# Kernel optimization log

Measured on AMD Instinct MI355X. Metric: run time of the kernel, lower is better.

Reference implementation:

```python
import jax, jax.numpy as jnp
import numpy as np

B, N, D, H = 8, 1024, 1024, 16
DK = D // H


def setup_inputs() -> dict:
    key = jax.random.key(0)
    ks = jax.random.split(key, 5)
    s_in = 1.0 / np.sqrt(D)
    return {
        "x": jax.random.normal(ks[0], (B, N, D), dtype=jnp.float32),
        "w_qkv": jax.random.uniform(ks[1], (D, 3 * D), jnp.float32, -s_in, s_in),
        "b_qkv": jax.random.uniform(ks[2], (3 * D,), jnp.float32, -s_in, s_in),
        "w_proj": jax.random.uniform(ks[3], (D, D), jnp.float32, -s_in, s_in),
        "b_proj": jax.random.uniform(ks[4], (D,), jnp.float32, -s_in, s_in),
    }


def reference(x, w_qkv, b_qkv, w_proj, b_proj):
    # x: (B, N, D)
    qkv = x @ w_qkv + b_qkv                      # (B, N, 3D)
    q, k, v = jnp.split(qkv, 3, axis=-1)
    # reshape to (B, H, N, DK)
    def heads(t):
        return t.reshape(B, N, H, DK).transpose(0, 2, 1, 3)
    q, k, v = heads(q), heads(k), heads(v)
    scale = 1.0 / np.sqrt(DK).astype(np.float32)
    scores = jnp.einsum("bhnd,bhmd->bhnm", q, k) * scale  # (B, H, N, N)
    attn = jax.nn.softmax(scores, axis=-1)
    out = jnp.einsum("bhnm,bhmd->bhnd", attn, v)          # (B, H, N, DK)
    out = out.transpose(0, 2, 1, 3).reshape(B, N, D)
    return out @ w_proj + b_proj
```

## Files before the change

kernel.cpp:

```cpp
#include <hip/hip_runtime.h>
#include <hip/hip_bf16.h>


#define BB 8
#define NN 1024
#define DD 1024
#define HH 16
#define DK 64
#define TOK (BB * NN)
#define QKVN (3 * DD)

typedef __attribute__((ext_vector_type(8))) short bf16x8;
typedef __attribute__((ext_vector_type(4))) float f32x4;
typedef __attribute__((ext_vector_type(4))) short short4v;
typedef __attribute__((ext_vector_type(4))) float float4v;

static __device__ __forceinline__ short f2bf(float f) {
  union { float f; unsigned u; } v; v.f = f;
  unsigned r = (v.u + 0x7FFFu + ((v.u >> 16) & 1u)) >> 16;
  return (short)r;
}
static __device__ __forceinline__ short f2bf_rn(float f) {
  __hip_bfloat16 h(f);
  short s;
  __builtin_memcpy(&s, &h, 2);
  return s;
}
static __device__ __forceinline__ float fexp2(float x) {
#if __has_builtin(__builtin_amdgcn_exp2f)
  return __builtin_amdgcn_exp2f(x);
#else
  return __expf(x * 0.69314718056f);
#endif
}

static __device__ __forceinline__ void gload_lds16(const short* g, short* lds, int lane) {
#if __has_builtin(__builtin_amdgcn_global_load_lds)
  __builtin_amdgcn_global_load_lds((const __attribute__((address_space(1))) void*)g,
                                   (__attribute__((address_space(3))) void*)lds, 16, 0, 0);
#else
  ((bf16x8*)lds)[lane] = *(const bf16x8*)g;
#endif
}

static __device__ __forceinline__ void block_barrier() {
  asm volatile("" ::: "memory");
  __builtin_amdgcn_s_barrier();
  asm volatile("" ::: "memory");
}

__global__ __launch_bounds__(256) void cast_f32_bf16(const float* __restrict__ in,
                                                     short* __restrict__ out, long n) {
  long i = ((long)blockIdx.x * blockDim.x + threadIdx.x) * 4;
  if (i >= n) return;
  float4v v = *(const float4v*)(in + i);
  short4v o;
  o[0] = f2bf(v[0]); o[1] = f2bf(v[1]); o[2] = f2bf(v[2]); o[3] = f2bf(v[3]);
  *(short4v*)(out + i) = o;
}

__global__ __launch_bounds__(256) void transpose_cast(const float* __restrict__ in,
                                                      short* __restrict__ out,
                                                      int rows, int cols) {
  __shared__ float tile[32][33];
  int bx = blockIdx.x * 32;
  int by = blockIdx.y * 32;
  int tx = threadIdx.x, ty = threadIdx.y;
#pragma unroll
  for (int q = 0; q < 4; q++)
    tile[ty + 8 * q][tx] = in[(long)(by + ty + 8 * q) * cols + bx + tx];
  __syncthreads();
#pragma unroll
  for (int q = 0; q < 4; q++)
    out[(long)(bx + ty + 8 * q) * rows + by + tx] = f2bf(tile[tx][ty + 8 * q]);
}

__global__ __launch_bounds__(512, 2) void gemm256(const short* __restrict__ A,
                                                  const short* __restrict__ Bt,
                                                  const float* __restrict__ bias,
                                                  short* __restrict__ Cqk,
                                                  int M, int N, int K, int ldc) {
  __shared__ __align__(16) short lds[2][2][2][128 * 64];
  const int tid = threadIdx.x;
  const int wid = tid >> 6, lane = tid & 63;
  const int r = lane & 15, g = lane >> 4;
  const int wm = wid >> 2, wn = wid & 3;

  const int nwg = gridDim.x * gridDim.y;
  const int flat = blockIdx.y * gridDim.x + blockIdx.x;
  const int swz = (flat & 7) * (nwg >> 3) + (flat >> 3);
  const int bx = swz % gridDim.x, by = swz / gridDim.x;
  const long tileM = (long)by * 256, tileN = (long)bx * 256;

  f32x4 acc[8][4] = {};

  const int sc = ((lane & 7) ^ ((lane >> 3) & 7)) * 8;
  const int srl = lane >> 3;

  const int akc0 = ((0 + g) ^ (r & 7)) * 8;
  const int akc1 = ((4 + g) ^ (r & 7)) * 8;
  const int bn0 = (wn & 1) * 64;
  const int bhh = wn >> 1;

#define STAGEA(buf, h, Tt)                                                          \
  {                                                                                 \
    _Pragma("unroll") for (int j = 0; j < 2; j++)                                   \
      gload_lds16(A + (tileM + (h) * 128 + wid * 16 + j * 8 + srl) * (long)K +      \
                      (Tt) * 64 + sc,                                               \
                  &lds[buf][0][h][(wid * 2 + j) * 512], lane);                      \
  }
#define STAGEB(buf, h, Tt)                                                          \
  {                                                                                 \
    _Pragma("unroll") for (int j = 0; j < 2; j++)                                   \
      gload_lds16(Bt + (tileN + (h) * 128 + wid * 16 + j * 8 + srl) * (long)K +     \
                      (Tt) * 64 + sc,                                               \
                  &lds[buf][1][h][(wid * 2 + j) * 512], lane);                      \
  }
#define READ_A(q, p)                                                                \
  af[0][0] = *(const bf16x8*)&lds[q][0][wm][((p) * 32 + r) * 64 + akc0];            \
  af[0][1] = *(const bf16x8*)&lds[q][0][wm][((p) * 32 + r) * 64 + akc1];            \
  af[1][0] = *(const bf16x8*)&lds[q][0][wm][((p) * 32 + 16 + r) * 64 + akc0];       \
  af[1][1] = *(const bf16x8*)&lds[q][0][wm][((p) * 32 + 16 + r) * 64 + akc1];
#define READ_B(q)                                                                   \
  {                                                                                 \
    const short* Bh = &lds[q][1][bhh][0];                                           \
    _Pragma("unroll") for (int fn = 0; fn < 4; fn++) {                              \
      bf[fn][0] = *(const bf16x8*)&Bh[(bn0 + fn * 16 + r) * 64 + akc0];             \
      bf[fn][1] = *(const bf16x8*)&Bh[(bn0 + fn * 16 + r) * 64 + akc1];             \
    }                                                                               \
  }
#define WAITL()                                                                     \
  asm volatile("s_waitcnt lgkmcnt(0)" ::: "memory");                                \
  __builtin_amdgcn_sched_barrier(0);
#define MFMA_P(p)                                                                   \
  __builtin_amdgcn_s_setprio(1);                                                    \
  _Pragma("unroll") for (int fmi = 0; fmi < 2; fmi++)                               \
      _Pragma("unroll") for (int fn = 0; fn < 4; fn++) {                            \
    acc[2 * (p) + fmi][fn] = __builtin_amdgcn_mfma_f32_16x16x32_bf16(               \
        af[fmi][0], bf[fn][0], acc[2 * (p) + fmi][fn], 0, 0, 0);                    \
    acc[2 * (p) + fmi][fn] = __builtin_amdgcn_mfma_f32_16x16x32_bf16(               \
        af[fmi][1], bf[fn][1], acc[2 * (p) + fmi][fn], 0, 0, 0);                    \
  }                                                                                 \
  __builtin_amdgcn_s_setprio(0);

  const int NT = K >> 6;
  const int NIT = NT >> 1;

  STAGEA(0, 0, 0); STAGEA(0, 1, 0); STAGEB(0, 0, 0); STAGEB(0, 1, 0);
  STAGEB(1, 0, 1); STAGEB(1, 1, 1);
  asm volatile("s_waitcnt vmcnt(4)" ::: "memory");
  block_barrier();

  for (int i = 0; i < NIT; ++i) {
    const int t1 = 2 * i + 1, t2 = 2 * i + 2, t3 = 2 * i + 3;
    const bool full = (i < NIT - 1);
    bf16x8 af[2][2], bf[4][2];

    READ_A(0, 0); READ_B(0);
    STAGEA(1, 0, t1);
    block_barrier(); WAITL(); MFMA_P(0); block_barrier();

    READ_A(0, 1);
    STAGEA(1, 1, t1);
    block_barrier(); WAITL(); MFMA_P(1); block_barrier();

    READ_A(0, 2);
    if (full) STAGEB(0, 0, t2);
    block_barrier(); WAITL(); MFMA_P(2); block_barrier();

    READ_A(0, 3);
    if (full) STAGEB(0, 1, t2);
    if (full) asm volatile("s_waitcnt vmcnt(4)" ::: "memory");
    else      asm volatile("s_waitcnt vmcnt(0)" ::: "memory");
    block_barrier(); WAITL(); MFMA_P(3); block_barrier();

    READ_A(1, 0); READ_B(1);
    if (full) STAGEA(0, 0, t2);
    block_barrier(); WAITL(); MFMA_P(0); block_barrier();

    READ_A(1, 1);
    if (full) STAGEA(0, 1, t2);
    block_barrier(); WAITL(); MFMA_P(1); block_barrier();

    READ_A(1, 2);
    if (full) STAGEB(1, 0, t3);
    block_barrier(); WAITL(); MFMA_P(2); block_barrier();

    READ_A(1, 3);
    if (full) STAGEB(1, 1, t3);
    if (full) asm volatile("s_waitcnt vmcnt(4)" ::: "memory");
    block_barrier(); WAITL(); MFMA_P(3); block_barrier();
  }
#undef STAGEA
#undef STAGEB
#undef READ_A
#undef READ_B
#undef WAITL
#undef MFMA_P

#pragma unroll
  for (int fm = 0; fm < 8; fm++) {
    long rowb = tileM + wm * 128 + fm * 16 + g * 4;
#pragma unroll
    for (int fn = 0; fn < 4; fn++) {
      long cn = tileN + wn * 64 + fn * 16 + r;
      float bv = bias[cn];
      Cqk[(rowb + 0) * ldc + cn] = f2bf(acc[fm][fn][0] + bv);
      Cqk[(rowb + 1) * ldc + cn] = f2bf(acc[fm][fn][1] + bv);
      Cqk[(rowb + 2) * ldc + cn] = f2bf(acc[fm][fn][2] + bv);
      Cqk[(rowb + 3) * ldc + cn] = f2bf(acc[fm][fn][3] + bv);
    }
  }
}

template <int MODE>
__global__ __launch_bounds__(256) void gemm_bt(const short* __restrict__ A,
                                               const short* __restrict__ Bt,
                                               const float* __restrict__ bias,
                                               void* __restrict__ Cout,
                                               short* __restrict__ vT,
                                               int M, int N, int K, int ldc) {
  __shared__ __align__(16) short As[2][128 * 32];
  __shared__ __align__(16) short Bs[2][128 * 32];
  const int tid = threadIdx.x;
  const int w = tid >> 6, lane = tid & 63;
  const int r = lane & 15, g = lane >> 4;
  const int wm = w >> 1, wn = w & 1;

  const int nwg = gridDim.x * gridDim.y;
  const int flat = blockIdx.y * gridDim.x + blockIdx.x;
  const int swz = (flat & 7) * (nwg >> 3) + (flat >> 3);
  const int bx = swz % gridDim.x, by = swz / gridDim.x;

  const long tileM = (long)by * 128;
  const long tileN = (long)bx * 128;

  f32x4 acc[4][4] = {};

  const int rowInChunk = lane >> 2;
  const int colOff = ((lane & 3) ^ ((lane >> 3) & 3)) * 8;
  const int rdChunk = (g ^ ((r >> 1) & 3)) * 8;

  const int nt = K >> 5;
#pragma unroll
  for (int issue = 0; issue < 2; ++issue) {
    int c = w * 2 + issue;
    gload_lds16(A + (tileM + c * 16 + rowInChunk) * (long)K + colOff, &As[0][c * 512], lane);
    gload_lds16(Bt + (tileN + c * 16 + rowInChunk) * (long)K + colOff, &Bs[0][c * 512], lane);
  }
  __syncthreads();

  for (int t = 0; t < nt; ++t) {
    const int cur = t & 1;
    if (t + 1 < nt) {
      const int k0 = (t + 1) << 5;
#pragma unroll
      for (int issue = 0; issue < 2; ++issue) {
        int c = w * 2 + issue;
        gload_lds16(A + (tileM + c * 16 + rowInChunk) * (long)K + k0 + colOff,
                    &As[cur ^ 1][c * 512], lane);
        gload_lds16(Bt + (tileN + c * 16 + rowInChunk) * (long)K + k0 + colOff,
                    &Bs[cur ^ 1][c * 512], lane);
      }
    }

    bf16x8 a[4], b[4];
#pragma unroll
    for (int i = 0; i < 4; i++)
      a[i] = *(const bf16x8*)&As[cur][(wm * 64 + i * 16 + r) * 32 + rdChunk];
#pragma unroll
    for (int i = 0; i < 4; i++)
      b[i] = *(const bf16x8*)&Bs[cur][(wn * 64 + i * 16 + r) * 32 + rdChunk];
#pragma unroll
    for (int i = 0; i < 4; i++)
#pragma unroll
      for (int ii = 0; ii < 4; ii++)
        acc[i][ii] = __builtin_amdgcn_mfma_f32_16x16x32_bf16(a[i], b[ii], acc[i][ii], 0, 0, 0);

    __syncthreads();
  }

#pragma unroll
  for (int i = 0; i < 4; i++) {
    long rowb = tileM + wm * 64 + i * 16 + g * 4;
#pragma unroll
    for (int ii = 0; ii < 4; ii++) {
      long cn = tileN + wn * 64 + ii * 16 + r;
      float bv = bias[cn];
      float v0 = acc[i][ii][0] + bv;
      float v1 = acc[i][ii][1] + bv;
      float v2 = acc[i][ii][2] + bv;
      float v3 = acc[i][ii][3] + bv;
      if constexpr (MODE == 0) {
        float* C = (float*)Cout;
        C[(rowb + 0) * ldc + cn] = v0;
        C[(rowb + 1) * ldc + cn] = v1;
        C[(rowb + 2) * ldc + cn] = v2;
        C[(rowb + 3) * ldc + cn] = v3;
      } else {
        int hc = (int)cn;
        int b = (int)(rowb >> 10);
        int n0 = (int)(rowb & 1023);
        int pos = (n0 & ~31) + 8 * ((n0 >> 2) & 3) + 4 * ((n0 >> 4) & 1);
        long va = ((long)(b * 16 + (hc >> 6)) * 64 + (hc & 63)) * 1024 + pos;
        short4v sv;
        sv[0] = f2bf(v0); sv[1] = f2bf(v1); sv[2] = f2bf(v2); sv[3] = f2bf(v3);
        *(short4v*)&vT[va] = sv;
      }
    }
  }
}

__global__ __launch_bounds__(512) void attn_kernel(const short* __restrict__ qk,
                                                   const short* __restrict__ vT,
                                                   short* __restrict__ attn_out) {
  __shared__ __align__(16) short Ks[64 * 64];
  __shared__ __align__(16) short Vs[64 * 64];

  const int nwg = gridDim.x * gridDim.y;
  const int flat = blockIdx.y * gridDim.x + blockIdx.x;
  const int swz = (flat & 7) * (nwg >> 3) + (flat >> 3);
  const int bh = swz >> 2;
  const int qt = swz & 3;

  const int bb = bh >> 4, h = bh & 15;
  const int tid = threadIdx.x;
  const int wid = tid >> 6, lane = tid & 63;
  const int r = lane & 15, g = lane >> 4;
  const int qbase = qt * 256 + wid * 32;
  const int RS = 2048;
  const long base = (long)bb * NN * RS;
  const short* Qp = qk + base + h * 64;
  const short* Kp = qk + base + DD + h * 64;
  const short* vTh = vT + (long)bh * 64 * 1024;

  const int srow = 8 * wid + (lane >> 3);
  const int sj = (lane & 7) ^ (lane >> 3);

  bf16x8 qf[2][2];
#pragma unroll
  for (int qg = 0; qg < 2; qg++) {
    const short* qrow = Qp + (long)(qbase + 16 * qg + r) * RS;
    qf[qg][0] = *(const bf16x8*)(qrow + 8 * g);
    qf[qg][1] = *(const bf16x8*)(qrow + 32 + 8 * g);
  }

  const float C = 0.18033688f;
  float m2[2] = {-3e38f, -3e38f}, lsum[2] = {0.0f, 0.0f};
  f32x4 o[2][4] = {};

  for (int kv0 = 0; kv0 < NN; kv0 += 64) {
    __syncthreads();
    gload_lds16(Kp + (long)(kv0 + srow) * RS + sj * 8, &Ks[wid * 512], lane);
    gload_lds16(vTh + (long)srow * 1024 + kv0 + sj * 8, &Vs[wid * 512], lane);
    __syncthreads();

    bf16x8 kf[2][2][2];
#pragma unroll
    for (int c = 0; c < 2; c++)
#pragma unroll
      for (int u = 0; u < 2; u++) {
        int krow = 32 * c + 16 * u + r;
#pragma unroll
        for (int s = 0; s < 2; s++)
          kf[c][u][s] = *(const bf16x8*)&Ks[krow * 64 + (((4 * s + g) ^ (r & 7)) * 8)];
      }

    bf16x8 pf[2][2];
#pragma unroll
    for (int qg = 0; qg < 2; qg++) {
      f32x4 s[2][2];
      __builtin_amdgcn_s_setprio(1);
#pragma unroll
      for (int c = 0; c < 2; c++)
#pragma unroll
        for (int u = 0; u < 2; u++) {
          f32x4 t = {};
          t = __builtin_amdgcn_mfma_f32_16x16x32_bf16(kf[c][u][0], qf[qg][0], t, 0, 0, 0);
          s[c][u] = __builtin_amdgcn_mfma_f32_16x16x32_bf16(kf[c][u][1], qf[qg][1], t, 0, 0, 0);
        }
      __builtin_amdgcn_s_setprio(0);

      float s16[16];
#pragma unroll
      for (int c = 0; c < 2; c++)
#pragma unroll
        for (int j = 0; j < 4; j++) {
          s16[8 * c + j] = s[c][0][j];
          s16[8 * c + 4 + j] = s[c][1][j];
        }

      float t8[8];
#pragma unroll
      for (int j = 0; j < 8; j++) t8[j] = fmaxf(s16[j], s16[j + 8]);
#pragma unroll
      for (int j = 0; j < 4; j++) t8[j] = fmaxf(t8[j], t8[j + 4]);
      float tmax = fmaxf(fmaxf(t8[0], t8[1]), fmaxf(t8[2], t8[3]));
      tmax = fmaxf(tmax, __shfl_xor(tmax, 16));
      tmax = fmaxf(tmax, __shfl_xor(tmax, 32));
      float tm2 = tmax * C;

      if (!__all(tm2 <= m2[qg] + 11.5416f)) {
        float mnew = fmaxf(m2[qg], tm2);
        float corr = fexp2(m2[qg] - mnew);
#pragma unroll
        for (int t = 0; t < 4; t++)
#pragma unroll
          for (int j = 0; j < 4; j++) o[qg][t][j] *= corr;
        lsum[qg] *= corr;
        m2[qg] = mnew;
      }

      float pv[16];
#pragma unroll
      for (int j = 0; j < 16; j++) pv[j] = fexp2(fmaf(s16[j], C, -m2[qg]));
      float s8[8];
#pragma unroll
      for (int j = 0; j < 8; j++) s8[j] = pv[j] + pv[j + 8];
#pragma unroll
      for (int j = 0; j < 4; j++) s8[j] = s8[j] + s8[j + 4];
      float ps = (s8[0] + s8[1]) + (s8[2] + s8[3]);
      ps += __shfl_xor(ps, 16);
      ps += __shfl_xor(ps, 32);
      lsum[qg] += ps;
#pragma unroll
      for (int c = 0; c < 2; c++)
#pragma unroll
        for (int j = 0; j < 8; j++) pf[qg][c][j] = f2bf_rn(pv[8 * c + j]);
    }

#pragma unroll
    for (int t = 0; t < 4; t++) {
      int vrow = 16 * t + r;
#pragma unroll
      for (int c = 0; c < 2; c++) {
        bf16x8 vt = *(const bf16x8*)&Vs[vrow * 64 + (((4 * c + g) ^ (r & 7)) * 8)];
        __builtin_amdgcn_s_setprio(1);
        o[0][t] = __builtin_amdgcn_mfma_f32_16x16x32_bf16(vt, pf[0][c], o[0][t], 0, 0, 0);
        o[1][t] = __builtin_amdgcn_mfma_f32_16x16x32_bf16(vt, pf[1][c], o[1][t], 0, 0, 0);
        __builtin_amdgcn_s_setprio(0);
      }
    }
  }

#pragma unroll
  for (int qg = 0; qg < 2; qg++) {
    float inv = 1.0f / lsum[qg];
    long orow = (long)(bb * NN + qbase + 16 * qg + r) * DD + h * 64;
#pragma unroll
    for (int t = 0; t < 4; t++) {
      short4v svv;
#pragma unroll
      for (int j = 0; j < 4; j++) svv[j] = f2bf(o[qg][t][j] * inv);
      *(short4v*)&attn_out[orow + 16 * t + 4 * g] = svv;
    }
  }
}

extern "C" void kernel_launch(void* const* d_in, const int* in_sizes, int n_in,
                              void* d_out, int out_size, void* d_ws, size_t ws_size,
                              hipStream_t stream) {
  const float* x = (const float*)d_in[0];
  const float* w_qkv = (const float*)d_in[1];
  const float* b_qkv = (const float*)d_in[2];
  const float* w_proj = (const float*)d_in[3];
  const float* b_proj = (const float*)d_in[4];
  float* out = (float*)d_out;

  short* ws = (short*)d_ws;
  short* xb = ws;
  short* wqkvT = xb + (long)TOK * DD;
  short* wprojT = wqkvT + (long)QKVN * DD;
  short* qkb = wprojT + (long)DD * DD;
  short* vT = qkb + (long)TOK * 2048;
  short* attn = vT + (long)TOK * DD;

  cast_f32_bf16<<<(TOK * DD) / (256 * 4), 256, 0, stream>>>(x, xb, (long)TOK * DD);
  transpose_cast<<<dim3(QKVN / 32, DD / 32), dim3(32, 8), 0, stream>>>(w_qkv, wqkvT, DD, QKVN);
  transpose_cast<<<dim3(DD / 32, DD / 32), dim3(32, 8), 0, stream>>>(w_proj, wprojT, DD, DD);

  gemm256<<<dim3(2048 / 256, TOK / 256), 512, 0, stream>>>(xb, wqkvT, b_qkv, qkb,
                                                           TOK, 2048, DD, 2048);

  gemm_bt<2><<<dim3(DD / 128, TOK / 128), 256, 0, stream>>>(
      xb, wqkvT + (long)2048 * DD, b_qkv + 2048, nullptr, vT, TOK, DD, DD, 0);

  attn_kernel<<<dim3(4, BB * HH), 512, 0, stream>>>(qkb, vT, attn);

  gemm_bt<0><<<dim3(DD / 128, TOK / 128), 256, 0, stream>>>(attn, wprojT, b_proj, out, nullptr,
                                                            TOK, DD, DD, DD);
}
```

Measured before the change: 158.0 us.

## Double-buffer K/V tiles in attention and compute row sums via MFMA

The attention kernel now keeps two LDS buffers for K and V. The next tile is loaded while the current one is computed, which removes one barrier per iteration and hides global load latency. The softmax denominator is no longer built from VALU adds and cross-lane shuffles; an MFMA with an all-ones operand accumulates it from the bf16-rounded probabilities. This doubles LDS use and adds MFMA work, and the denominator now matches the bf16-rounded weights actually used in the PV product.

```diff
diff --git a/kernel.cpp b/kernel.cpp
--- a/kernel.cpp
+++ b/kernel.cpp
@@ -314,8 +314,10 @@
 __global__ __launch_bounds__(512) void attn_kernel(const short* __restrict__ qk,
                                                    const short* __restrict__ vT,
                                                    short* __restrict__ attn_out) {
-  __shared__ __align__(16) short Ks[64 * 64];
-  __shared__ __align__(16) short Vs[64 * 64];
+  __shared__ __align__(16) short K0s[64 * 64];
+  __shared__ __align__(16) short V0s[64 * 64];
+  __shared__ __align__(16) short K1s[64 * 64];
+  __shared__ __align__(16) short V1s[64 * 64];
 
   const int nwg = gridDim.x * gridDim.y;
   const int flat = blockIdx.y * gridDim.x + blockIdx.x;
@@ -345,107 +347,107 @@
     qf[qg][1] = *(const bf16x8*)(qrow + 32 + 8 * g);
   }
 
+  bf16x8 ones;
+#pragma unroll
+  for (int j = 0; j < 8; j++) ones[j] = (short)0x3F80;
+
   const float C = 0.18033688f;
-  float m2[2] = {-3e38f, -3e38f}, lsum[2] = {0.0f, 0.0f};
+  float m2[2] = {-3e38f, -3e38f};
   f32x4 o[2][4] = {};
-
-  for (int kv0 = 0; kv0 < NN; kv0 += 64) {
-    __syncthreads();
-    gload_lds16(Kp + (long)(kv0 + srow) * RS + sj * 8, &Ks[wid * 512], lane);
-    gload_lds16(vTh + (long)srow * 1024 + kv0 + sj * 8, &Vs[wid * 512], lane);
-    __syncthreads();
-
-    bf16x8 kf[2][2][2];
-#pragma unroll
-    for (int c = 0; c < 2; c++)
-#pragma unroll
-      for (int u = 0; u < 2; u++) {
-        int krow = 32 * c + 16 * u + r;
-#pragma unroll
-        for (int s = 0; s < 2; s++)
-          kf[c][u][s] = *(const bf16x8*)&Ks[krow * 64 + (((4 * s + g) ^ (r & 7)) * 8)];
-      }
-
-    bf16x8 pf[2][2];
-#pragma unroll
-    for (int qg = 0; qg < 2; qg++) {
-      f32x4 s[2][2];
-      __builtin_amdgcn_s_setprio(1);
-#pragma unroll
-      for (int c = 0; c < 2; c++)
-#pragma unroll
-        for (int u = 0; u < 2; u++) {
-          f32x4 t = {};
-          t = __builtin_amdgcn_mfma_f32_16x16x32_bf16(kf[c][u][0], qf[qg][0], t, 0, 0, 0);
-          s[c][u] = __builtin_amdgcn_mfma_f32_16x16x32_bf16(kf[c][u][1], qf[qg][1], t, 0, 0, 0);
-        }
-      __builtin_amdgcn_s_setprio(0);
-
-      float s16[16];
-#pragma unroll
-      for (int c = 0; c < 2; c++)
-#pragma unroll
-        for (int j = 0; j < 4; j++) {
-          s16[8 * c + j] = s[c][0][j];
-          s16[8 * c + 4 + j] = s[c][1][j];
-        }
-
-      float t8[8];
-#pragma unroll
-      for (int j = 0; j < 8; j++) t8[j] = fmaxf(s16[j], s16[j + 8]);
-#pragma unroll
-      for (int j = 0; j < 4; j++) t8[j] = fmaxf(t8[j], t8[j + 4]);
-      float tmax = fmaxf(fmaxf(t8[0], t8[1]), fmaxf(t8[2], t8[3]));
-      tmax = fmaxf(tmax, __shfl_xor(tmax, 16));
-      tmax = fmaxf(tmax, __shfl_xor(tmax, 32));
-      float tm2 = tmax * C;
-
-      if (!__all(tm2 <= m2[qg] + 11.5416f)) {
-        float mnew = fmaxf(m2[qg], tm2);
-        float corr = fexp2(m2[qg] - mnew);
-#pragma unroll
-        for (int t = 0; t < 4; t++)
-#pragma unroll
-          for (int j = 0; j < 4; j++) o[qg][t][j] *= corr;
-        lsum[qg] *= corr;
-        m2[qg] = mnew;
-      }
-
-      float pv[16];
-#pragma unroll
-      for (int j = 0; j < 16; j++) pv[j] = fexp2(fmaf(s16[j], C, -m2[qg]));
-      float s8[8];
-#pragma unroll
-      for (int j = 0; j < 8; j++) s8[j] = pv[j] + pv[j + 8];
-#pragma unroll
-      for (int j = 0; j < 4; j++) s8[j] = s8[j] + s8[j + 4];
-      float ps = (s8[0] + s8[1]) + (s8[2] + s8[3]);
-      ps += __shfl_xor(ps, 16);
-      ps += __shfl_xor(ps, 32);
-      lsum[qg] += ps;
-#pragma unroll
-      for (int c = 0; c < 2; c++)
-#pragma unroll
-        for (int j = 0; j < 8; j++) pf[qg][c][j] = f2bf_rn(pv[8 * c + j]);
+  f32x4 osum[2] = {};
+
+#define STAGE(kv, Kd, Vd)                                                     \
+  gload_lds16(Kp + (long)((kv) + srow) * RS + sj * 8, &Kd[wid * 512], lane);  \
+  gload_lds16(vTh + (long)srow * 1024 + (kv) + sj * 8, &Vd[wid * 512], lane);
+
+#define COMPUTE(Ksb, Vsb)                                                              \
+  do {                                                                                 \
+    bf16x8 kf[2][2][2];                                                                \
+    _Pragma("unroll") for (int c = 0; c < 2; c++)                                      \
+    _Pragma("unroll") for (int u = 0; u < 2; u++) {                                    \
+      int krow = 32 * c + 16 * u + r;                                                  \
+      _Pragma("unroll") for (int s2 = 0; s2 < 2; s2++)                                 \
+        kf[c][u][s2] =                                                                 \
+            *(const bf16x8*)&Ksb[krow * 64 + (((4 * s2 + g) ^ (r & 7)) * 8)];          \
+    }                                                                                  \
+    bf16x8 pf[2][2];                                                                   \
+    _Pragma("unroll") for (int qg = 0; qg < 2; qg++) {                                 \
+      f32x4 sacc[2][2];                                                                \
+      __builtin_amdgcn_s_setprio(1);                                                   \
+      _Pragma("unroll") for (int c = 0; c < 2; c++)                                    \
+      _Pragma("unroll") for (int u = 0; u < 2; u++) {                                  \
+        f32x4 tt = {};                                                                 \
+        tt = __builtin_amdgcn_mfma_f32_16x16x32_bf16(kf[c][u][0], qf[qg][0], tt, 0, 0, 0); \
+        sacc[c][u] =                                                                   \
+            __builtin_amdgcn_mfma_f32_16x16x32_bf16(kf[c][u][1], qf[qg][1], tt, 0, 0, 0); \
+      }                                                                                \
+      __builtin_amdgcn_s_setprio(0);                                                   \
+      float s16[16];                                                                   \
+      _Pragma("unroll") for (int c = 0; c < 2; c++)                                    \
+      _Pragma("unroll") for (int j = 0; j < 4; j++) {                                  \
+        s16[8 * c + j] = sacc[c][0][j];                                                \
+        s16[8 * c + 4 + j] = sacc[c][1][j];                                            \
+      }                                                                                \
+      float t8[8];                                                                     \
+      _Pragma("unroll") for (int j = 0; j < 8; j++) t8[j] = fmaxf(s16[j], s16[j + 8]); \
+      _Pragma("unroll") for (int j = 0; j < 4; j++) t8[j] = fmaxf(t8[j], t8[j + 4]);   \
+      float tmax = fmaxf(fmaxf(t8[0], t8[1]), fmaxf(t8[2], t8[3]));                    \
+      tmax = fmaxf(tmax, __shfl_xor(tmax, 16));                                        \
+      tmax = fmaxf(tmax, __shfl_xor(tmax, 32));                                        \
+      float tm2 = tmax * C;                                                            \
+      if (!__all(tm2 <= m2[qg] + 11.5416f)) {                                          \
+        float mnew = fmaxf(m2[qg], tm2);                                               \
+        float corr = fexp2(m2[qg] - mnew);                                             \
+        _Pragma("unroll") for (int t = 0; t < 4; t++)                                  \
+        _Pragma("unroll") for (int j = 0; j < 4; j++) o[qg][t][j] *= corr;             \
+        osum[qg][0] *= corr; osum[qg][1] *= corr;                                      \
+        osum[qg][2] *= corr; osum[qg][3] *= corr;                                      \
+        m2[qg] = mnew;                                                                 \
+      }                                                                                \
+      float pvv[16];                                                                   \
+      _Pragma("unroll") for (int j = 0; j < 16; j++)                                   \
+        pvv[j] = fexp2(fmaf(s16[j], C, -m2[qg]));                                      \
+      _Pragma("unroll") for (int c = 0; c < 2; c++)                                    \
+      _Pragma("unroll") for (int j = 0; j < 8; j++)                                    \
+        pf[qg][c][j] = f2bf_rn(pvv[8 * c + j]);                                        \
+      osum[qg] = __builtin_amdgcn_mfma_f32_16x16x32_bf16(ones, pf[qg][0], osum[qg], 0, 0, 0); \
+      osum[qg] = __builtin_amdgcn_mfma_f32_16x16x32_bf16(ones, pf[qg][1], osum[qg], 0, 0, 0); \
+    }                                                                                  \
+    _Pragma("unroll") for (int t = 0; t < 4; t++) {                                    \
+      int vrow = 16 * t + r;                                                           \
+      _Pragma("unroll") for (int c = 0; c < 2; c++) {                                  \
+        bf16x8 vt = *(const bf16x8*)&Vsb[vrow * 64 + (((4 * c + g) ^ (r & 7)) * 8)];   \
+        __builtin_amdgcn_s_setprio(1);                                                 \
+        o[0][t] = __builtin_amdgcn_mfma_f32_16x16x32_bf16(vt, pf[0][c], o[0][t], 0, 0, 0); \
+        o[1][t] = __builtin_amdgcn_mfma_f32_16x16x32_bf16(vt, pf[1][c], o[1][t], 0, 0, 0); \
+        __builtin_amdgcn_s_setprio(0);                                                 \
+      }                                                                                \
+    }                                                                                  \
+  } while (0)
+
+  STAGE(0, K0s, V0s);
+  asm volatile("s_waitcnt vmcnt(0)" ::: "memory");
+  block_barrier();
+
+  for (int it = 0; it < NN / 128; ++it) {
+    STAGE(128 * it + 64, K1s, V1s);
+    COMPUTE(K0s, V0s);
+    asm volatile("s_waitcnt vmcnt(0)" ::: "memory");
+    block_barrier();
+
+    if (it + 1 < NN / 128) {
+      STAGE(128 * (it + 1), K0s, V0s);
     }
-
-#pragma unroll
-    for (int t = 0; t < 4; t++) {
-      int vrow = 16 * t + r;
-#pragma unroll
-      for (int c = 0; c < 2; c++) {
-        bf16x8 vt = *(const bf16x8*)&Vs[vrow * 64 + (((4 * c + g) ^ (r & 7)) * 8)];
-        __builtin_amdgcn_s_setprio(1);
-        o[0][t] = __builtin_amdgcn_mfma_f32_16x16x32_bf16(vt, pf[0][c], o[0][t], 0, 0, 0);
-        o[1][t] = __builtin_amdgcn_mfma_f32_16x16x32_bf16(vt, pf[1][c], o[1][t], 0, 0, 0);
-        __builtin_amdgcn_s_setprio(0);
-      }
-    }
-  }
+    COMPUTE(K1s, V1s);
+    asm volatile("s_waitcnt vmcnt(0)" ::: "memory");
+    block_barrier();
+  }
+#undef STAGE
+#undef COMPUTE
 
 #pragma unroll
   for (int qg = 0; qg < 2; qg++) {
-    float inv = 1.0f / lsum[qg];
+    float inv = 1.0f / osum[qg][0];
     long orow = (long)(bb * NN + qbase + 16 * qg + r) * DD + h * 64;
 #pragma unroll
     for (int t = 0; t < 4; t++) {
```

Measured after the change: 166.3 us. 1.05x slower.
